# Optimization experiments

Measured on AMD Instinct MI355X. Metric: run time of the kernel, lower is better.

Reference implementation:

```python
import jax, jax.numpy as jnp
import numpy as np

B, L, S, H, E = 4, 2048, 2048, 8, 64

def setup_inputs() -> dict:
    key = jax.random.key(0)
    kq, kk, kv, kt, kd = jax.random.split(key, 5)
    return {
        "queries": jax.random.normal(kq, (B, L, H, E), dtype=jnp.float32),
        "keys": jax.random.normal(kk, (B, S, H, E), dtype=jnp.float32),
        "values": jax.random.normal(kv, (B, S, H, E), dtype=jnp.float32),
        "attn_mask": jnp.zeros((1,), dtype=bool),
        "tau": jax.random.uniform(kt, (B, 1), dtype=jnp.float32),
        "delta": jax.random.normal(kd, (B, 1), dtype=jnp.float32),
    }

def reference(queries, keys, values, attn_mask, tau, delta):
    # queries: [B,L,H,E], keys: [B,S,H,E], values: [B,S,H,D]
    Bq, Lq, Hq, Eq = queries.shape
    scale = 1.0 / jnp.sqrt(jnp.float32(Eq))
    scores = jnp.einsum('blhe,bshe->bhls', queries, keys)  # [B,H,L,S]
    scores = scores * tau.reshape(Bq, 1, 1, 1)             # per-batch tau scale
    scores = scores + delta.reshape(Bq, 1, 1, 1)           # per-batch delta bias
    A = jax.nn.softmax(scale * scores, axis=-1)            # dropout is identity at eval
    V = jnp.einsum('bhls,bshd->blhd', A, values)           # [B,L,H,D]
    return V
```

## Files before the change

kernel.cpp:

```cpp
#include <hip/hip_runtime.h>
#include <hip/hip_bf16.h>
#include <stdint.h>

#define LL 2048
#define SS 2048
#define HH 8
#define EE 64
#define RSG 512

typedef float v4f  __attribute__((ext_vector_type(4)));
typedef float v16f __attribute__((ext_vector_type(16)));
typedef short s4v  __attribute__((ext_vector_type(4)));
typedef short s8v  __attribute__((ext_vector_type(8)));

__device__ __forceinline__ short f2bf(float f) {
    unsigned u = __float_as_uint(f);
    u = (u + 0x7fffu + ((u >> 16) & 1u)) >> 16;
    return (short)u;
}

__device__ __forceinline__ s4v pack4bf(float a, float b, float c, float d) {
    float2 ab = make_float2(a, b), cd = make_float2(c, d);
    __hip_bfloat162 r0 = __float22bfloat162_rn(ab);
    __hip_bfloat162 r1 = __float22bfloat162_rn(cd);
    s4v r;
    __builtin_memcpy(&r, &r0, 4);
    __builtin_memcpy(((char*)&r) + 4, &r1, 4);
    return r;
}

__global__ __launch_bounds__(256)
void dsattn_prep(const float* __restrict__ kk, const float* __restrict__ vv,
                 short* __restrict__ kbf, short* __restrict__ vimg)
{
    __shared__ float T[64][68];
    const int t = threadIdx.x;
    const int blk = blockIdx.x;
    if (blk < 1024) {
        const float* src = kk + (size_t)blk * 4096;
        short* dst = kbf + (size_t)blk * 4096;
        #pragma unroll
        for (int c = 0; c < 4; ++c) {
            v4f d = *(const v4f*)(src + (c * 256 + t) * 4);
            *(s4v*)(dst + (c * 256 + t) * 4) = pack4bf(d[0], d[1], d[2], d[3]);
        }
    } else {
        const int vb = blk - 1024;
        const int b = vb >> 8, h = (vb >> 5) & 7, ts = vb & 31;
        const float* vp = vv + ((size_t)b * SS + ts * 64) * RSG + h * EE;
        #pragma unroll
        for (int c = 0; c < 4; ++c) {
            int idx = c * 256 + t, s = idx >> 4, e0 = (idx & 15) << 2;
            *(v4f*)&T[s][e0] = *(const v4f*)(vp + (size_t)s * RSG + e0);
        }
        __syncthreads();
        short* dst = vimg + (size_t)vb * 4096;
        #pragma unroll
        for (int half = 0; half < 2; ++half) {
            int ci = half * 256 + t;
            int e = ci >> 3, pos = ci & 7;
            int c = pos ^ (e & 7);
            int sbase = 16 * (c >> 1) + 4 * (c & 1);
            s8v ov;
            #pragma unroll
            for (int j = 0; j < 8; ++j) {
                int s = sbase + 8 * (j >> 2) + (j & 3);
                ov[j] = f2bf(T[s][e]);
            }
            *(s8v*)(dst + ci * 8) = ov;
        }
    }
}

__global__ __launch_bounds__(256, 2)
void dsattn_main(const float* __restrict__ q, const short* __restrict__ kbf,
                 const short* __restrict__ vimg, const float* __restrict__ tau,
                 float* __restrict__ out)
{
    __shared__ short KV[4][8192];

    const int t    = threadIdx.x;
    const int lane = t & 63;
    const int w    = t >> 6;
    const int l31  = lane & 31;
    const int hi   = lane >> 5;

    const int hw = blockIdx.x;
    const int wu = (hw & 7) * 64 + (hw >> 3);
    const int mt = wu & 15;
    const int h  = (wu >> 4) & 7;
    const int b  = wu >> 7;

    const float scf = 0.125f * 1.44269504088896f * tau[b];

    s8v qf[4];
    {
        const float* qb = q + ((size_t)b * LL + (size_t)mt * 128 + w * 32 + l31) * RSG
                            + h * EE + 8 * hi;
        #pragma unroll
        for (int ks = 0; ks < 4; ++ks) {
            v4f a0 = *(const v4f*)(qb + 16 * ks);
            v4f a1 = *(const v4f*)(qb + 16 * ks + 4);
            s4v p0 = pack4bf(a0[0] * scf, a0[1] * scf, a0[2] * scf, a0[3] * scf);
            s4v p1 = pack4bf(a1[0] * scf, a1[1] * scf, a1[2] * scf, a1[3] * scf);
            s8v f;
            #pragma unroll
            for (int j = 0; j < 4; ++j) { f[j] = p0[j]; f[4 + j] = p1[j]; }
            qf[ks] = f;
        }
    }

    const char* gsrc;
    int jstr, tstr;
    if (w < 2) {
        int i = w * 256 + lane;
        int row = i >> 3;
        int c = (i & 7) ^ (row & 7);
        gsrc = (const char*)(kbf + (size_t)b * (SS * RSG) + h * EE) + row * (RSG * 2) + c * 16;
        jstr = 8 * RSG * 2;
        tstr = 64 * RSG * 2;
    } else {
        int i2 = (w - 2) * 256 + lane;
        gsrc = (const char*)(vimg + (((size_t)b * HH + h) * 32) * 4096) + i2 * 16;
        jstr = 1024; tstr = 8192;
    }

    #define STAGE(slot)                                                                   \
        {                                                                                 \
            _Pragma("unroll")                                                             \
            for (int j = 0; j < 4; ++j) {                                                 \
                __builtin_amdgcn_global_load_lds(                                         \
                    (const __attribute__((address_space(1))) unsigned*)(gsrc + j * jstr), \
                    (__attribute__((address_space(3))) unsigned*)&KV[slot][w * 2048 + j * 512], \
                    16, 0, 0);                                                            \
            }                                                                             \
            gsrc += tstr;                                                                 \
        }

    v16f oacc[2];
    #pragma unroll
    for (int mb = 0; mb < 2; ++mb)
        #pragma unroll
        for (int r = 0; r < 16; ++r) oacc[mb][r] = 0.0f;
    float rsum = 0.0f;

    const int xo = l31 & 7;
    const int rbase = l31 * 64;
    int kpos[4];
    #pragma unroll
    for (int ks = 0; ks < 4; ++ks) kpos[ks] = (((hi + 2 * ks) & 7) ^ xo) * 8;

    STAGE(0);
    STAGE(1);
    STAGE(2);

    #pragma unroll 4
    for (int it = 0; it < 32; ++it) {
        const int p = it & 3;

        __builtin_amdgcn_sched_barrier(0);
        if (it <= 29)      asm volatile("s_waitcnt vmcnt(8)" ::: "memory");
        else if (it == 30) asm volatile("s_waitcnt vmcnt(4)" ::: "memory");
        else               asm volatile("s_waitcnt vmcnt(0)" ::: "memory");
        __builtin_amdgcn_s_barrier();
        __builtin_amdgcn_sched_barrier(0);

        if (it <= 28) STAGE((it + 3) & 3);

        const short* Kp = &KV[p][0];
        const short* Vp = &KV[p][4096];

        v16f st[2];
        #pragma unroll
        for (int mb = 0; mb < 2; ++mb) {
            v16f z;
            #pragma unroll
            for (int r = 0; r < 16; ++r) z[r] = 0.0f;
            #pragma unroll
            for (int ks = 0; ks < 4; ++ks) {
                s8v kf = *(const s8v*)&Kp[mb * 2048 + rbase + kpos[ks]];
                z = __builtin_amdgcn_mfma_f32_32x32x16_bf16(kf, qf[ks], z, 0, 0, 0);
            }
            st[mb] = z;
        }

        #pragma unroll
        for (int mb = 0; mb < 2; ++mb)
            #pragma unroll
            for (int r = 0; r < 16; ++r)
                st[mb][r] = __builtin_amdgcn_exp2f(st[mb][r]);
        float s0 = 0.f, s1 = 0.f;
        #pragma unroll
        for (int r = 0; r < 16; ++r) { s0 += st[0][r]; s1 += st[1][r]; }
        rsum += s0 + s1;

        s8v pf[4];
        #pragma unroll
        for (int tt = 0; tt < 4; ++tt) {
            int o = 8 * (tt & 1);
            const v16f& sv = st[tt >> 1];
            s4v lo = pack4bf(sv[o + 0], sv[o + 1], sv[o + 2], sv[o + 3]);
            s4v hs = pack4bf(sv[o + 4], sv[o + 5], sv[o + 6], sv[o + 7]);
            s8v f;
            #pragma unroll
            for (int j = 0; j < 4; ++j) { f[j] = lo[j]; f[4 + j] = hs[j]; }
            pf[tt] = f;
        }

        #pragma unroll
        for (int mb = 0; mb < 2; ++mb) {
            v16f acc = oacc[mb];
            #pragma unroll
            for (int ks = 0; ks < 4; ++ks) {
                s8v vf = *(const s8v*)&Vp[mb * 2048 + rbase + kpos[ks]];
                acc = __builtin_amdgcn_mfma_f32_32x32x16_bf16(vf, pf[ks], acc, 0, 0, 0);
            }
            oacc[mb] = acc;
        }
    }

    rsum += __shfl_xor(rsum, 32);
    const float inv = 1.0f / rsum;
    float* ob = out + ((size_t)b * LL + (size_t)mt * 128 + w * 32 + l31) * RSG + h * EE;
    #pragma unroll
    for (int mb = 0; mb < 2; ++mb)
        #pragma unroll
        for (int rq = 0; rq < 4; ++rq) {
            int e0 = 32 * mb + 8 * rq + 4 * hi;
            v4f o4 = { oacc[mb][4 * rq + 0] * inv, oacc[mb][4 * rq + 1] * inv,
                       oacc[mb][4 * rq + 2] * inv, oacc[mb][4 * rq + 3] * inv };
            *(v4f*)(ob + e0) = o4;
        }
}

extern "C" void kernel_launch(void* const* d_in, const int* in_sizes, int n_in,
                              void* d_out, int out_size, void* d_ws, size_t ws_size,
                              hipStream_t stream) {
    const float* q     = (const float*)d_in[0];
    const float* k     = (const float*)d_in[1];
    const float* v     = (const float*)d_in[2];
    const float* tau   = (const float*)d_in[4];
    float* out = (float*)d_out;

    short* kbf  = (short*)d_ws;
    short* vimg = kbf + (size_t)4 * SS * RSG;

    dsattn_prep<<<dim3(2048), dim3(256), 0, stream>>>(k, v, kbf, vimg);
    dsattn_main<<<dim3(512), dim3(256), 0, stream>>>(q, kbf, vimg, tau, out);
}
```

Measured before the change: 137.0 us.

## Software-pipeline QK and PV across iterations to overlap exp with MFMA

Restructures the attention main loop so each iteration computes QK scores for the current tile and the PV product for the previous tile, then does the exp and bf16 pack. The intent is to let the independent MFMA chains run alongside the transcendental and packing work instead of serializing on them. To make room for the extra live tile, prefetch depth drops from three staged tiles to two, with adjusted waitcnt values, a prologue and an epilogue. This may expose more memory latency and raises register pressure.

```diff
diff --git a/kernel.cpp b/kernel.cpp
--- a/kernel.cpp
+++ b/kernel.cpp
@@ -150,74 +150,100 @@
     #pragma unroll
     for (int ks = 0; ks < 4; ++ks) kpos[ks] = (((hi + 2 * ks) & 7) ^ xo) * 8;
 
+    asm volatile("s_waitcnt vmcnt(0)" ::: "memory");
+    __builtin_amdgcn_sched_barrier(0);
     STAGE(0);
     STAGE(1);
-    STAGE(2);
+
+    #define QK_TILE(P_)                                                                   \
+        {                                                                                 \
+            const short* Kp = &KV[P_][0];                                                 \
+            _Pragma("unroll")                                                             \
+            for (int mb = 0; mb < 2; ++mb) {                                              \
+                v16f z;                                                                   \
+                _Pragma("unroll")                                                         \
+                for (int r = 0; r < 16; ++r) z[r] = 0.0f;                                 \
+                _Pragma("unroll")                                                         \
+                for (int ks = 0; ks < 4; ++ks) {                                          \
+                    s8v kf = *(const s8v*)&Kp[mb * 2048 + rbase + kpos[ks]];              \
+                    z = __builtin_amdgcn_mfma_f32_32x32x16_bf16(kf, qf[ks], z, 0, 0, 0);  \
+                }                                                                         \
+                st[mb] = z;                                                               \
+            }                                                                             \
+        }
+
+    #define EXP_PACK()                                                                    \
+        {                                                                                 \
+            _Pragma("unroll")                                                             \
+            for (int mb = 0; mb < 2; ++mb)                                                \
+                _Pragma("unroll")                                                         \
+                for (int r = 0; r < 16; ++r)                                              \
+                    st[mb][r] = __builtin_amdgcn_exp2f(st[mb][r]);                        \
+            float s0 = 0.f, s1 = 0.f;                                                     \
+            _Pragma("unroll")                                                             \
+            for (int r = 0; r < 16; ++r) { s0 += st[0][r]; s1 += st[1][r]; }              \
+            rsum += s0 + s1;                                                              \
+            _Pragma("unroll")                                                             \
+            for (int tt = 0; tt < 4; ++tt) {                                              \
+                int o = 8 * (tt & 1);                                                     \
+                const v16f& sv = st[tt >> 1];                                             \
+                s4v lo = pack4bf(sv[o + 0], sv[o + 1], sv[o + 2], sv[o + 3]);             \
+                s4v hs = pack4bf(sv[o + 4], sv[o + 5], sv[o + 6], sv[o + 7]);             \
+                s8v f;                                                                    \
+                _Pragma("unroll")                                                         \
+                for (int j = 0; j < 4; ++j) { f[j] = lo[j]; f[4 + j] = hs[j]; }           \
+                pfp[tt] = f;                                                              \
+            }                                                                             \
+        }
+
+    #define PV_TILE(P_)                                                                   \
+        {                                                                                 \
+            const short* Vp = &KV[P_][4096];                                              \
+            _Pragma("unroll")                                                             \
+            for (int mb = 0; mb < 2; ++mb) {                                              \
+                v16f acc = oacc[mb];                                                      \
+                _Pragma("unroll")                                                         \
+                for (int ks = 0; ks < 4; ++ks) {                                          \
+                    s8v vf = *(const s8v*)&Vp[mb * 2048 + rbase + kpos[ks]];              \
+                    acc = __builtin_amdgcn_mfma_f32_32x32x16_bf16(vf, pfp[ks], acc, 0, 0, 0); \
+                }                                                                         \
+                oacc[mb] = acc;                                                           \
+            }                                                                             \
+        }
+
+    s8v pfp[4];
+
+    {
+        __builtin_amdgcn_sched_barrier(0);
+        asm volatile("s_waitcnt vmcnt(4)" ::: "memory");
+        __builtin_amdgcn_s_barrier();
+        __builtin_amdgcn_sched_barrier(0);
+        STAGE(2);
+        v16f st[2];
+        QK_TILE(0);
+        EXP_PACK();
+    }
 
     #pragma unroll 4
-    for (int it = 0; it < 32; ++it) {
-        const int p = it & 3;
-
-        __builtin_amdgcn_sched_barrier(0);
-        if (it <= 29)      asm volatile("s_waitcnt vmcnt(8)" ::: "memory");
-        else if (it == 30) asm volatile("s_waitcnt vmcnt(4)" ::: "memory");
-        else               asm volatile("s_waitcnt vmcnt(0)" ::: "memory");
+    for (int it = 1; it < 32; ++it) {
+        const int p   = it & 3;
+        const int pm1 = (it - 1) & 3;
+
+        __builtin_amdgcn_sched_barrier(0);
+        if (it <= 30) asm volatile("s_waitcnt vmcnt(4)" ::: "memory");
+        else          asm volatile("s_waitcnt vmcnt(0)" ::: "memory");
         __builtin_amdgcn_s_barrier();
         __builtin_amdgcn_sched_barrier(0);
 
-        if (it <= 28) STAGE((it + 3) & 3);
-
-        const short* Kp = &KV[p][0];
-        const short* Vp = &KV[p][4096];
+        if (it <= 29) STAGE((it + 2) & 3);
 
         v16f st[2];
-        #pragma unroll
-        for (int mb = 0; mb < 2; ++mb) {
-            v16f z;
-            #pragma unroll
-            for (int r = 0; r < 16; ++r) z[r] = 0.0f;
-            #pragma unroll
-            for (int ks = 0; ks < 4; ++ks) {
-                s8v kf = *(const s8v*)&Kp[mb * 2048 + rbase + kpos[ks]];
-                z = __builtin_amdgcn_mfma_f32_32x32x16_bf16(kf, qf[ks], z, 0, 0, 0);
-            }
-            st[mb] = z;
-        }
-
-        #pragma unroll
-        for (int mb = 0; mb < 2; ++mb)
-            #pragma unroll
-            for (int r = 0; r < 16; ++r)
-                st[mb][r] = __builtin_amdgcn_exp2f(st[mb][r]);
-        float s0 = 0.f, s1 = 0.f;
-        #pragma unroll
-        for (int r = 0; r < 16; ++r) { s0 += st[0][r]; s1 += st[1][r]; }
-        rsum += s0 + s1;
-
-        s8v pf[4];
-        #pragma unroll
-        for (int tt = 0; tt < 4; ++tt) {
-            int o = 8 * (tt & 1);
-            const v16f& sv = st[tt >> 1];
-            s4v lo = pack4bf(sv[o + 0], sv[o + 1], sv[o + 2], sv[o + 3]);
-            s4v hs = pack4bf(sv[o + 4], sv[o + 5], sv[o + 6], sv[o + 7]);
-            s8v f;
-            #pragma unroll
-            for (int j = 0; j < 4; ++j) { f[j] = lo[j]; f[4 + j] = hs[j]; }
-            pf[tt] = f;
-        }
-
-        #pragma unroll
-        for (int mb = 0; mb < 2; ++mb) {
-            v16f acc = oacc[mb];
-            #pragma unroll
-            for (int ks = 0; ks < 4; ++ks) {
-                s8v vf = *(const s8v*)&Vp[mb * 2048 + rbase + kpos[ks]];
-                acc = __builtin_amdgcn_mfma_f32_32x32x16_bf16(vf, pf[ks], acc, 0, 0, 0);
-            }
-            oacc[mb] = acc;
-        }
-    }
+        QK_TILE(p);
+        PV_TILE(pm1);
+        EXP_PACK();
+    }
+
+    PV_TILE(3);
 
     rsum += __shfl_xor(rsum, 32);
     const float inv = 1.0f / rsum;
```

Measured after the change: 545.9 us. 299% more time.

## Pre-tile K into per-head fragment-ordered image matching MFMA read layout

Applied to the files above, without the earlier changes.

The prep kernel now transposes K through shared memory into a contiguous per-(batch, head, tile) image, ordered so each MFMA lane's 8-element fragment sits at ks*1024 + mb*256 + lane offset. V gets the same linear fragment ordering, with no XOR swizzle. The main kernel can then stream both K and V with simple contiguous global-to-LDS copies and read fragments at linear offsets, which removes the strided K gather and the swizzle arithmetic. The trade-off is a costlier K prep pass, the loss of the swizzle that avoided LDS bank conflicts (lanes now read consecutive 16-byte chunks), and an added vmcnt(0) wait before the prologue.

```diff
diff --git a/kernel.cpp b/kernel.cpp
--- a/kernel.cpp
+++ b/kernel.cpp
@@ -31,18 +31,30 @@
 
 __global__ __launch_bounds__(256)
 void dsattn_prep(const float* __restrict__ kk, const float* __restrict__ vv,
-                 short* __restrict__ kbf, short* __restrict__ vimg)
+                 short* __restrict__ kimg, short* __restrict__ vimg)
 {
     __shared__ float T[64][68];
     const int t = threadIdx.x;
     const int blk = blockIdx.x;
     if (blk < 1024) {
-        const float* src = kk + (size_t)blk * 4096;
-        short* dst = kbf + (size_t)blk * 4096;
+        const int vb = blk;
+        const int b = vb >> 8, h = (vb >> 5) & 7, ts = vb & 31;
+        const float* kp = kk + ((size_t)b * SS + ts * 64) * RSG + h * EE;
         #pragma unroll
         for (int c = 0; c < 4; ++c) {
-            v4f d = *(const v4f*)(src + (c * 256 + t) * 4);
-            *(s4v*)(dst + (c * 256 + t) * 4) = pack4bf(d[0], d[1], d[2], d[3]);
+            int idx = c * 256 + t, s = idx >> 4, e0 = (idx & 15) << 2;
+            *(v4f*)&T[s][e0] = *(const v4f*)(kp + (size_t)s * RSG + e0);
+        }
+        __syncthreads();
+        short* dst = kimg + (size_t)vb * 4096;
+        #pragma unroll
+        for (int half = 0; half < 2; ++half) {
+            int ci = half * 256 + t;
+            int echunk = ci >> 6, srow = ci & 63;
+            s8v ov;
+            #pragma unroll
+            for (int j = 0; j < 8; ++j) ov[j] = f2bf(T[srow][echunk * 8 + j]);
+            *(s8v*)(dst + ci * 8) = ov;
         }
     } else {
         const int vb = blk - 1024;
@@ -58,8 +70,7 @@
         #pragma unroll
         for (int half = 0; half < 2; ++half) {
             int ci = half * 256 + t;
-            int e = ci >> 3, pos = ci & 7;
-            int c = pos ^ (e & 7);
+            int c = ci >> 6, e = ci & 63;
             int sbase = 16 * (c >> 1) + 4 * (c & 1);
             s8v ov;
             #pragma unroll
@@ -73,7 +84,7 @@
 }
 
 __global__ __launch_bounds__(256, 2)
-void dsattn_main(const float* __restrict__ q, const short* __restrict__ kbf,
+void dsattn_main(const float* __restrict__ q, const short* __restrict__ kimg,
                  const short* __restrict__ vimg, const float* __restrict__ tau,
                  float* __restrict__ out)
 {
@@ -111,18 +122,10 @@
     }
 
     const char* gsrc;
-    int jstr, tstr;
-    if (w < 2) {
-        int i = w * 256 + lane;
-        int row = i >> 3;
-        int c = (i & 7) ^ (row & 7);
-        gsrc = (const char*)(kbf + (size_t)b * (SS * RSG) + h * EE) + row * (RSG * 2) + c * 16;
-        jstr = 8 * RSG * 2;
-        tstr = 64 * RSG * 2;
-    } else {
-        int i2 = (w - 2) * 256 + lane;
-        gsrc = (const char*)(vimg + (((size_t)b * HH + h) * 32) * 4096) + i2 * 16;
-        jstr = 1024; tstr = 8192;
+    {
+        const size_t pan = (size_t)((b * 8 + h) * 32) * 8192;
+        if (w < 2) gsrc = (const char*)kimg + pan + w * 4096 + lane * 16;
+        else       gsrc = (const char*)vimg + pan + (w - 2) * 4096 + lane * 16;
     }
 
     #define STAGE(slot)                                                                   \
@@ -130,11 +133,11 @@
             _Pragma("unroll")                                                             \
             for (int j = 0; j < 4; ++j) {                                                 \
                 __builtin_amdgcn_global_load_lds(                                         \
-                    (const __attribute__((address_space(1))) unsigned*)(gsrc + j * jstr), \
+                    (const __attribute__((address_space(1))) unsigned*)(gsrc + j * 1024), \
                     (__attribute__((address_space(3))) unsigned*)&KV[slot][w * 2048 + j * 512], \
                     16, 0, 0);                                                            \
             }                                                                             \
-            gsrc += tstr;                                                                 \
+            gsrc += 8192;                                                                 \
         }
 
     v16f oacc[2];
@@ -144,12 +147,10 @@
         for (int r = 0; r < 16; ++r) oacc[mb][r] = 0.0f;
     float rsum = 0.0f;
 
-    const int xo = l31 & 7;
-    const int rbase = l31 * 64;
-    int kpos[4];
-    #pragma unroll
-    for (int ks = 0; ks < 4; ++ks) kpos[ks] = (((hi + 2 * ks) & 7) ^ xo) * 8;
-
+    const int rb = hi * 512 + l31 * 8;
+
+    asm volatile("s_waitcnt vmcnt(0)" ::: "memory");
+    __builtin_amdgcn_sched_barrier(0);
     STAGE(0);
     STAGE(1);
     STAGE(2);
@@ -178,7 +179,7 @@
             for (int r = 0; r < 16; ++r) z[r] = 0.0f;
             #pragma unroll
             for (int ks = 0; ks < 4; ++ks) {
-                s8v kf = *(const s8v*)&Kp[mb * 2048 + rbase + kpos[ks]];
+                s8v kf = *(const s8v*)&Kp[ks * 1024 + mb * 256 + rb];
                 z = __builtin_amdgcn_mfma_f32_32x32x16_bf16(kf, qf[ks], z, 0, 0, 0);
             }
             st[mb] = z;
@@ -212,7 +213,7 @@
             v16f acc = oacc[mb];
             #pragma unroll
             for (int ks = 0; ks < 4; ++ks) {
-                s8v vf = *(const s8v*)&Vp[mb * 2048 + rbase + kpos[ks]];
+                s8v vf = *(const s8v*)&Vp[ks * 1024 + mb * 256 + rb];
                 acc = __builtin_amdgcn_mfma_f32_32x32x16_bf16(vf, pf[ks], acc, 0, 0, 0);
             }
             oacc[mb] = acc;
@@ -242,9 +243,9 @@
     const float* tau   = (const float*)d_in[4];
     float* out = (float*)d_out;
 
-    short* kbf  = (short*)d_ws;
-    short* vimg = kbf + (size_t)4 * SS * RSG;
-
-    dsattn_prep<<<dim3(2048), dim3(256), 0, stream>>>(k, v, kbf, vimg);
-    dsattn_main<<<dim3(512), dim3(256), 0, stream>>>(q, kbf, vimg, tau, out);
-}
+    short* kimg = (short*)d_ws;
+    short* vimg = kimg + (size_t)4 * SS * RSG;
+
+    dsattn_prep<<<dim3(2048), dim3(256), 0, stream>>>(k, v, kimg, vimg);
+    dsattn_main<<<dim3(512), dim3(256), 0, stream>>>(q, kimg, vimg, tau, out);
+}
```

New measurement: 136.2 us. No clear change (-0.5%).
